# Kernel tuning notes

Measured on AMD Instinct MI355X. Metric: run time of the kernel, lower is better.

## Reference

```python
import jax, jax.numpy as jnp
import numpy as np

N_IN = 1024
N_OUT = 1024
BATCH = 8192
N_GRID = 10  # grid_points = linspace(-1, 1, 10); 9 segments
LN_EPS = 1e-5


def setup_inputs() -> dict:
    key = jax.random.key(0)
    k = jax.random.split(key, 6)
    return {
        "x": jax.random.normal(k[0], (BATCH, N_IN), dtype=jnp.float32),
        "weights": jax.random.normal(k[1], (N_OUT, N_IN), dtype=jnp.float32) * (1.0 / np.sqrt(N_IN)),
        "biases": jax.random.normal(k[2], (N_OUT,), dtype=jnp.float32),
        "slopes": jax.random.normal(k[3], (N_OUT, N_IN, N_GRID - 1), dtype=jnp.float32) * 0.05,
        "intercepts": jax.random.normal(k[4], (N_OUT, N_IN, N_GRID - 1), dtype=jnp.float32) * 0.05,
        "prelu_weight": jnp.full((1,), 0.25, dtype=jnp.float32),
    }


def reference(x, weights, biases, slopes, intercepts, prelu_weight):
    grid = jnp.linspace(-1.0, 1.0, N_GRID, dtype=x.dtype)
    n_seg = N_GRID - 1

    # base branch: GELU (exact, matching torch nn.GELU default) then linear
    b_out = jax.nn.gelu(x, approximate=False) @ weights.T + biases  # [B, n_out]

    # segment index per (sample, input feature)
    pos = (x[..., None] - grid) >= 0  # [B, n_in, N_GRID]
    seg = jnp.clip(jnp.sum(pos.astype(jnp.int32), axis=-1) - 1, 0, n_seg - 1)  # [B, n_in]

    # Faithful to torch.gather semantics: only slopes[:, 0, :] / intercepts[:, 0, :]
    # are read (index dim-2 has size 1 -> j==0). The piecewise sum over n_in then
    # reduces to segment-sums of x and segment counts contracted with those slices.
    onehot = jax.nn.one_hot(seg, n_seg, dtype=x.dtype)  # [B, n_in, n_seg]
    seg_x = jnp.einsum('bis,bi->bs', onehot, x)          # sum of x per segment
    seg_cnt = jnp.sum(onehot, axis=1)                    # count per segment
    slopes0 = slopes[:, 0, :]        # [n_out, n_seg]
    icpt0 = intercepts[:, 0, :]      # [n_out, n_seg]
    lin = seg_x @ slopes0.T + seg_cnt @ icpt0.T          # [B, n_out]

    y = b_out + lin
    # LayerNorm over n_out, no affine
    mu = jnp.mean(y, axis=-1, keepdims=True)
    var = jnp.mean(jnp.square(y - mu), axis=-1, keepdims=True)
    yn = (y - mu) * jax.lax.rsqrt(var + LN_EPS)
    # PReLU with single shared weight
    return jnp.where(yn >= 0, yn, prelu_weight * yn)
```

## Files before the change

kernel.cpp:

```cpp
#include <hip/hip_runtime.h>
#include <hip/hip_fp8.h>

#define N_IN 1024
#define N_OUT 1024
#define BATCHN 8192

typedef __attribute__((ext_vector_type(4))) int intx4;
typedef __attribute__((ext_vector_type(8))) int intx8;
typedef __attribute__((ext_vector_type(16))) float floatx16;

__device__ __forceinline__ unsigned int pk4_e4m3(float a, float b, float c,
                                                 float d) {
  int w = __builtin_amdgcn_cvt_pk_fp8_f32(a, b, 0, false);
  w = __builtin_amdgcn_cvt_pk_fp8_f32(c, d, w, true);
  return (unsigned int)w;
}
__device__ __forceinline__ float gelu_fast(float v) {
  float e = __builtin_amdgcn_exp2f(-2.4554443f * v);
  return v * __builtin_amdgcn_rcpf(1.0f + e);
}

#define ASYNC_CP16(gp, lp)                                                     \
  __builtin_amdgcn_global_load_lds(                                            \
      (const __attribute__((address_space(1))) unsigned int*)(gp),             \
      (__attribute__((address_space(3))) unsigned int*)(lp), 16, 0, 0)

__global__ __launch_bounds__(256) void prep_all(const float* __restrict__ x,
                                                unsigned char* __restrict__ g8,
                                                float2* __restrict__ seg2g,
                                                const float* __restrict__ W,
                                                unsigned char* __restrict__ Wb8,
                                                const float* __restrict__ slopes,
                                                const float* __restrict__ icpts,
                                                float* __restrict__ slt,
                                                float* __restrict__ ict) {
  const int b = blockIdx.x, t = threadIdx.x;
  if (b < BATCHN / 4) {
    const int lane = t & 63, w = t >> 6;
    const int r = b * 4 + w;
    const float* xr = x + (long)r * N_IN;
    unsigned int* grow = (unsigned int*)(g8 + (long)r * N_IN);
    const int sw = r & 7;
    float cumx[8], totx = 0.f;
    unsigned int cnt[8];
#pragma unroll
    for (int s = 0; s < 8; ++s) { cnt[s] = 0u; cumx[s] = 0.f; }
#pragma unroll
    for (int jc = 0; jc < 4; ++jc) {
      float4 v4 = ((const float4*)xr)[lane + 64 * jc];
      float vs[4] = {v4.x, v4.y, v4.z, v4.w};
      float gs[4];
#pragma unroll
      for (int e = 0; e < 4; ++e) {
        float v = vs[e];
        gs[e] = gelu_fast(v) * 4.0f;
        totx += v;
#pragma unroll
        for (int k = 0; k < 8; ++k) {
          bool m = v >= (-1.0f + (float)(k + 1) * (2.0f / 9.0f));
          cumx[k] += m ? v : 0.0f;
          cnt[k] += (unsigned int)__popcll(__ballot(m));
        }
      }
      const unsigned int pk = pk4_e4m3(gs[0], gs[1], gs[2], gs[3]);
      const int d = lane + 64 * jc;
      grow[(((d >> 2) ^ sw) << 2) | (d & 3)] = pk;
    }
#pragma unroll
    for (int off = 32; off > 0; off >>= 1) {
      totx += __shfl_xor(totx, off);
#pragma unroll
      for (int s = 0; s < 8; ++s) cumx[s] += __shfl_xor(cumx[s], off);
    }
    if (lane == 0) {
      seg2g[r * 9 + 0] = make_float2(totx - cumx[0], (float)(1024 - (int)cnt[0]));
#pragma unroll
      for (int s = 1; s < 8; ++s)
        seg2g[r * 9 + s] = make_float2(cumx[s - 1] - cumx[s],
                                       (float)((int)cnt[s - 1] - (int)cnt[s]));
      seg2g[r * 9 + 8] = make_float2(cumx[7], (float)cnt[7]);
    }
  } else if (b < BATCHN / 4 + N_OUT) {
    const int o = b - BATCHN / 4;
    float4 v = ((const float4*)(W + o * N_IN))[t];
    unsigned int pk =
        pk4_e4m3(v.x * 16.0f, v.y * 16.0f, v.z * 16.0f, v.w * 16.0f);
    const int kc = t >> 4;
    const int lh = (t >> 3) & 1;
    const int sec = (t >> 2) & 1;
    const int off = (t & 3) * 4;
    const int lane = lh * 32 + (o & 31);
    *(unsigned int*)(Wb8 + kc * 65536 + (o >> 5) * 2048 + sec * 1024 +
                     lane * 16 + off) = pk;
  } else {
    const int gb = b - (BATCHN / 4 + N_OUT);
    const int o = gb * 16 + (t >> 4);
    const int s = t & 15;
    if (s < 9) {
      slt[s * N_OUT + o] = slopes[(long)o * 9216 + s];
      ict[s * N_OUT + o] = icpts[(long)o * 9216 + s];
    }
  }
}

__global__ __launch_bounds__(1024) void gemm_ln(
    const unsigned char* __restrict__ g8, const unsigned char* __restrict__ Wb8,
    const float* __restrict__ biases, const float* __restrict__ slt,
    const float* __restrict__ ict, const float* __restrict__ prelu_w,
    const float2* __restrict__ seg2g, float* __restrict__ out) {
  __shared__ unsigned char lA[32 * 1024];
  __shared__ float2 seg2f[288];
  __shared__ float2 red[16][32];
  __shared__ float2 rowstat[32];

  const int t = threadIdx.x;
  const int lane = t & 63, w = t >> 6;
  const int l31 = lane & 31, lh = lane >> 5;
  const int r0 = blockIdx.x * 32;

#pragma unroll
  for (int j = 0; j < 2; ++j) {
    const int sg = t + 1024 * j;
    ASYNC_CP16(g8 + (long)r0 * 1024 + sg * 16, &lA[sg * 16]);
  }
  if (t < 288) seg2f[t] = seg2g[r0 * 9 + t];
  __syncthreads();

  const int nb = w * 64;
  floatx16 acc[2] = {};
  const unsigned char* aRow = lA + l31 * 1024;
  const int asw = l31 & 7;
  const unsigned char* bBase = Wb8 + (w * 2) * 2048 + lane * 16;

#define LOAD_A(ko, AF)                                                         \
  {                                                                            \
    const int c0 = ((ko) >> 4) + lh * 2;                                       \
    intx4 lo = *(const intx4*)(aRow + ((c0 ^ asw) << 4));                      \
    intx4 hi = *(const intx4*)(aRow + (((c0 + 1) ^ asw) << 4));                \
    AF[0] = lo[0]; AF[1] = lo[1]; AF[2] = lo[2]; AF[3] = lo[3];                \
    AF[4] = hi[0]; AF[5] = hi[1]; AF[6] = hi[2]; AF[7] = hi[3];                \
  }
#define LOAD_B(kc, ni, BF)                                                     \
  {                                                                            \
    const unsigned char* bp = bBase + (kc) * 65536 + (ni) * 2048;              \
    intx4 lo = *(const intx4*)bp;                                              \
    intx4 hi = *(const intx4*)(bp + 1024);                                     \
    BF[0] = lo[0]; BF[1] = lo[1]; BF[2] = lo[2]; BF[3] = lo[3];                \
    BF[4] = hi[0]; BF[5] = hi[1]; BF[6] = hi[2]; BF[7] = hi[3];                \
  }

  const int rot = ((blockIdx.x >> 3) & 7) * 2;
  for (int kt0 = 0; kt0 < 16; kt0 += 2) {
    const int kt = (kt0 + rot) & 15;
    intx8 a0, a1, b0[2], b1[2];
    LOAD_A(kt * 64, a0);
    LOAD_A(kt * 64 + 64, a1);
#pragma unroll
    for (int ni = 0; ni < 2; ++ni) LOAD_B(kt, ni, b0[ni]);
#pragma unroll
    for (int ni = 0; ni < 2; ++ni) LOAD_B(kt + 1, ni, b1[ni]);
    __builtin_amdgcn_s_setprio(1);
#pragma unroll
    for (int ni = 0; ni < 2; ++ni)
      acc[ni] = __builtin_amdgcn_mfma_scale_f32_32x32x64_f8f6f4(
          a0, b0[ni], acc[ni], 0, 0, 0, 0x7D7D7D7Du , 0,
          0x7B7B7B7Bu );
#pragma unroll
    for (int ni = 0; ni < 2; ++ni)
      acc[ni] = __builtin_amdgcn_mfma_scale_f32_32x32x64_f8f6f4(
          a1, b1[ni], acc[ni], 0, 0, 0, 0x7D7D7D7Du, 0, 0x7B7B7B7Bu);
    __builtin_amdgcn_s_setprio(0);
  }

  float bb[2], cs[2][9], ci[2][9];
#pragma unroll
  for (int ni = 0; ni < 2; ++ni) {
    const int c = nb + ni * 32 + l31;
    bb[ni] = biases[c];
#pragma unroll
    for (int s = 0; s < 9; ++s) {
      cs[ni][s] = slt[s * N_OUT + c];
      ci[ni][s] = ict[s * N_OUT + c];
    }
  }

#pragma unroll
  for (int rg = 0; rg < 16; ++rg) {
    const int rl = (rg & 3) + 8 * (rg >> 2) + 4 * lh;
    float2 sp[9];
#pragma unroll
    for (int s = 0; s < 9; ++s) sp[s] = seg2f[rl * 9 + s];
    float ssum = 0.f, qsum = 0.f;
#pragma unroll
    for (int ni = 0; ni < 2; ++ni) {
      float y = acc[ni][rg] + bb[ni];
#pragma unroll
      for (int s = 0; s < 9; ++s) y += sp[s].x * cs[ni][s] + sp[s].y * ci[ni][s];
      acc[ni][rg] = y;
      ssum += y;
      qsum += y * y;
    }
#pragma unroll
    for (int off = 16; off > 0; off >>= 1) {
      ssum += __shfl_xor(ssum, off);
      qsum += __shfl_xor(qsum, off);
    }
    if (l31 == 0) red[w][rl] = make_float2(ssum, qsum);
  }
  __syncthreads();
  if (t < 32) {
    float s = 0.f, q = 0.f;
#pragma unroll
    for (int wv = 0; wv < 16; ++wv) {
      float2 p = red[wv][t];
      s += p.x;
      q += p.y;
    }
    const float mu = s * (1.0f / 1024.0f);
    const float rstd = rsqrtf(q * (1.0f / 1024.0f) - mu * mu + 1e-5f);
    rowstat[t] = make_float2(mu, rstd);
  }
  const float pw = prelu_w[0];
  __syncthreads();
#pragma unroll
  for (int rg = 0; rg < 16; ++rg) {
    const int rl = (rg & 3) + 8 * (rg >> 2) + 4 * lh;
    const float2 ms = rowstat[rl];
    float* orow = out + (r0 + rl) * N_OUT;
#pragma unroll
    for (int ni = 0; ni < 2; ++ni) {
      float z = (acc[ni][rg] - ms.x) * ms.y;
      z = z >= 0.f ? z : pw * z;
      __builtin_nontemporal_store(z, &orow[nb + ni * 32 + l31]);
    }
  }
}

extern "C" void kernel_launch(void* const* d_in, const int* in_sizes, int n_in,
                              void* d_out, int out_size, void* d_ws, size_t ws_size,
                              hipStream_t stream) {
  const float* x = (const float*)d_in[0];
  const float* W = (const float*)d_in[1];
  const float* biases = (const float*)d_in[2];
  const float* slopes = (const float*)d_in[3];
  const float* icpts = (const float*)d_in[4];
  const float* prelu_w = (const float*)d_in[5];
  float* out = (float*)d_out;

  char* ws = (char*)d_ws;
  unsigned char* Wb8 = (unsigned char*)ws;
  float* slt = (float*)(ws + (2u << 20));
  float* ict = (float*)(ws + (2u << 20) + (64u << 10));
  unsigned char* g8 = (unsigned char*)(ws + (4u << 20));
  float2* seg2g = (float2*)(ws + (12u << 20));

  prep_all<<<BATCHN / 4 + N_OUT + 64, 256, 0, stream>>>(
      x, g8, seg2g, W, Wb8, slopes, icpts, slt, ict);
  gemm_ln<<<BATCHN / 32, 1024, 0, stream>>>(g8, Wb8, biases, slt, ict, prelu_w,
                                            seg2g, out);
}
```

Measured before the change: 165.8 us.

## Software-pipeline weight fragment loads across K-steps and prefetch before the LDS barrier

Restructures the GEMM main loop so the B (weight) fragments for the next K-chunk load into a second register set while the current chunk's MFMAs run. The first B fragments are now issued before the async A-tile copy and barrier, so global latency overlaps the LDS staging. The K rotation now covers every chunk offset rather than only even ones, and an amdgpu_waves_per_eu(4,4) hint caps register use for the occupancy implied by 1024-thread blocks. In exchange, live registers rise and the prefetch depth is only one step, so the compiler may spill or reorder differently.

```diff
diff --git a/kernel.cpp b/kernel.cpp
--- a/kernel.cpp
+++ b/kernel.cpp
@@ -103,7 +103,8 @@
   }
 }
 
-__global__ __launch_bounds__(1024) void gemm_ln(
+__global__ __launch_bounds__(1024)
+__attribute__((amdgpu_waves_per_eu(4, 4))) void gemm_ln(
     const unsigned char* __restrict__ g8, const unsigned char* __restrict__ Wb8,
     const float* __restrict__ biases, const float* __restrict__ slt,
     const float* __restrict__ ict, const float* __restrict__ prelu_w,
@@ -118,16 +119,7 @@
   const int l31 = lane & 31, lh = lane >> 5;
   const int r0 = blockIdx.x * 32;
 
-#pragma unroll
-  for (int j = 0; j < 2; ++j) {
-    const int sg = t + 1024 * j;
-    ASYNC_CP16(g8 + (long)r0 * 1024 + sg * 16, &lA[sg * 16]);
-  }
-  if (t < 288) seg2f[t] = seg2g[r0 * 9 + t];
-  __syncthreads();
-
   const int nb = w * 64;
-  floatx16 acc[2] = {};
   const unsigned char* aRow = lA + l31 * 1024;
   const int asw = l31 & 7;
   const unsigned char* bBase = Wb8 + (w * 2) * 2048 + lane * 16;
@@ -148,27 +140,43 @@
     BF[0] = lo[0]; BF[1] = lo[1]; BF[2] = lo[2]; BF[3] = lo[3];                \
     BF[4] = hi[0]; BF[5] = hi[1]; BF[6] = hi[2]; BF[7] = hi[3];                \
   }
-
-  const int rot = ((blockIdx.x >> 3) & 7) * 2;
-  for (int kt0 = 0; kt0 < 16; kt0 += 2) {
-    const int kt = (kt0 + rot) & 15;
-    intx8 a0, a1, b0[2], b1[2];
-    LOAD_A(kt * 64, a0);
-    LOAD_A(kt * 64 + 64, a1);
-#pragma unroll
-    for (int ni = 0; ni < 2; ++ni) LOAD_B(kt, ni, b0[ni]);
-#pragma unroll
-    for (int ni = 0; ni < 2; ++ni) LOAD_B(kt + 1, ni, b1[ni]);
+#define MFMA(AF, BF, C)                                                        \
+  __builtin_amdgcn_mfma_scale_f32_32x32x64_f8f6f4(                             \
+      AF, BF, C, 0, 0, 0, 0x7D7D7D7Du , 0, 0x7B7B7B7Bu )
+
+  const int rot = (blockIdx.x >> 3) & 15;
+  intx8 a0, a1, bA0, bA1, bB0, bB1;
+  LOAD_B(rot, 0, bA0);
+  LOAD_B(rot, 1, bA1);
+#pragma unroll
+  for (int j = 0; j < 2; ++j) {
+    const int sg = t + 1024 * j;
+    ASYNC_CP16(g8 + (long)r0 * 1024 + sg * 16, &lA[sg * 16]);
+  }
+  if (t < 288) seg2f[t] = seg2g[r0 * 9 + t];
+  __syncthreads();
+
+  floatx16 acc[2] = {};
+#pragma unroll
+  for (int j = 0; j < 16; j += 2) {
+    const int k0 = (j + rot) & 15;
+    const int k1 = (j + 1 + rot) & 15;
+    const int k2 = (j + 2 + rot) & 15;
+    LOAD_A(k0 * 64, a0);
+    LOAD_B(k1, 0, bB0);
+    LOAD_B(k1, 1, bB1);
     __builtin_amdgcn_s_setprio(1);
-#pragma unroll
-    for (int ni = 0; ni < 2; ++ni)
-      acc[ni] = __builtin_amdgcn_mfma_scale_f32_32x32x64_f8f6f4(
-          a0, b0[ni], acc[ni], 0, 0, 0, 0x7D7D7D7Du , 0,
-          0x7B7B7B7Bu );
-#pragma unroll
-    for (int ni = 0; ni < 2; ++ni)
-      acc[ni] = __builtin_amdgcn_mfma_scale_f32_32x32x64_f8f6f4(
-          a1, b1[ni], acc[ni], 0, 0, 0, 0x7D7D7D7Du, 0, 0x7B7B7B7Bu);
+    acc[0] = MFMA(a0, bA0, acc[0]);
+    acc[1] = MFMA(a0, bA1, acc[1]);
+    __builtin_amdgcn_s_setprio(0);
+    LOAD_A(k1 * 64, a1);
+    if (j < 14) {
+      LOAD_B(k2, 0, bA0);
+      LOAD_B(k2, 1, bA1);
+    }
+    __builtin_amdgcn_s_setprio(1);
+    acc[0] = MFMA(a1, bB0, acc[0]);
+    acc[1] = MFMA(a1, bB1, acc[1]);
     __builtin_amdgcn_s_setprio(0);
   }
 
```

New measurement: 165.6 us. Within noise of the previous version (-0.1%).

## Double-buffer W and activation k-tiles through LDS with async prefetch

Applied to the files above, without the earlier changes.

The GEMM main loop now stages each 64-wide k-tile of the FP8 weight matrix and the matching activation slice into one of two large LDS buffers, using async global-to-LDS copies issued two tiles ahead. Previously the weight fragments were read straight from global memory and the whole 32-row activation block was loaded once into LDS. The prep kernel's activation layout is changed to a k-tile-major, 4-way XOR-swizzled layout so each tile is one contiguous 2 KB chunk. The aim is to hide global latency behind MFMA work. In exchange it adds a block-wide barrier per k-tile and roughly 132 KB of LDS per block, which limits occupancy to one block per CU.

```diff
diff --git a/kernel.cpp b/kernel.cpp
--- a/kernel.cpp
+++ b/kernel.cpp
@@ -39,8 +39,9 @@
     const int lane = t & 63, w = t >> 6;
     const int r = b * 4 + w;
     const float* xr = x + (long)r * N_IN;
-    unsigned int* grow = (unsigned int*)(g8 + (long)r * N_IN);
-    const int sw = r & 7;
+    unsigned int* g32 = (unsigned int*)g8;
+    const int rb = r >> 5, rl = r & 31, sw3 = rl & 3;
+    const unsigned int rowbase = ((unsigned int)rb << 13) + (rl << 4);
     float cumx[8], totx = 0.f;
     unsigned int cnt[8];
 #pragma unroll
@@ -64,7 +65,10 @@
       }
       const unsigned int pk = pk4_e4m3(gs[0], gs[1], gs[2], gs[3]);
       const int d = lane + 64 * jc;
-      grow[(((d >> 2) ^ sw) << 2) | (d & 3)] = pk;
+      const int kt = d >> 4;
+      const int c = (d >> 2) & 3;
+      const int wd = d & 3;
+      g32[rowbase + (kt << 9) + ((c ^ sw3) << 2) + wd] = pk;
     }
 #pragma unroll
     for (int off = 32; off > 0; off >>= 1) {
@@ -108,7 +112,7 @@
     const float* __restrict__ biases, const float* __restrict__ slt,
     const float* __restrict__ ict, const float* __restrict__ prelu_w,
     const float2* __restrict__ seg2g, float* __restrict__ out) {
-  __shared__ unsigned char lA[32 * 1024];
+  __shared__ unsigned char pool[2][67584];
   __shared__ float2 seg2f[288];
   __shared__ float2 red[16][32];
   __shared__ float2 rowstat[32];
@@ -117,58 +121,58 @@
   const int lane = t & 63, w = t >> 6;
   const int l31 = lane & 31, lh = lane >> 5;
   const int r0 = blockIdx.x * 32;
-
-#pragma unroll
-  for (int j = 0; j < 2; ++j) {
-    const int sg = t + 1024 * j;
-    ASYNC_CP16(g8 + (long)r0 * 1024 + sg * 16, &lA[sg * 16]);
-  }
+  const int rot = (blockIdx.x >> 3) & 15;
+
+#define STAGE(p, kte)                                                          \
+  {                                                                            \
+    const unsigned char* bsrc = Wb8 + (kte) * 65536;                           \
+    _Pragma("unroll") for (int j = 0; j < 4; ++j) {                            \
+      const int sg = t + 1024 * j;                                             \
+      ASYNC_CP16(bsrc + sg * 16, &pool[p][sg * 16]);                           \
+    }                                                                          \
+    if (t < 128)                                                               \
+      ASYNC_CP16(g8 + ((long)blockIdx.x << 15) + (kte) * 2048 + t * 16,        \
+                 &pool[p][65536 + t * 16]);                                    \
+  }
+#define MFMA(AF, BF, C)                                                        \
+  __builtin_amdgcn_mfma_scale_f32_32x32x64_f8f6f4(                             \
+      AF, BF, C, 0, 0, 0, 0x7D7D7D7Du , 0, 0x7B7B7B7Bu )
+
+  STAGE(0, rot);
+  STAGE(1, (rot + 1) & 15);
   if (t < 288) seg2f[t] = seg2g[r0 * 9 + t];
   __syncthreads();
 
   const int nb = w * 64;
   floatx16 acc[2] = {};
-  const unsigned char* aRow = lA + l31 * 1024;
-  const int asw = l31 & 7;
-  const unsigned char* bBase = Wb8 + (w * 2) * 2048 + lane * 16;
-
-#define LOAD_A(ko, AF)                                                         \
-  {                                                                            \
-    const int c0 = ((ko) >> 4) + lh * 2;                                       \
-    intx4 lo = *(const intx4*)(aRow + ((c0 ^ asw) << 4));                      \
-    intx4 hi = *(const intx4*)(aRow + (((c0 + 1) ^ asw) << 4));                \
-    AF[0] = lo[0]; AF[1] = lo[1]; AF[2] = lo[2]; AF[3] = lo[3];                \
-    AF[4] = hi[0]; AF[5] = hi[1]; AF[6] = hi[2]; AF[7] = hi[3];                \
-  }
-#define LOAD_B(kc, ni, BF)                                                     \
-  {                                                                            \
-    const unsigned char* bp = bBase + (kc) * 65536 + (ni) * 2048;              \
-    intx4 lo = *(const intx4*)bp;                                              \
-    intx4 hi = *(const intx4*)(bp + 1024);                                     \
-    BF[0] = lo[0]; BF[1] = lo[1]; BF[2] = lo[2]; BF[3] = lo[3];                \
-    BF[4] = hi[0]; BF[5] = hi[1]; BF[6] = hi[2]; BF[7] = hi[3];                \
-  }
-
-  const int rot = ((blockIdx.x >> 3) & 7) * 2;
-  for (int kt0 = 0; kt0 < 16; kt0 += 2) {
-    const int kt = (kt0 + rot) & 15;
-    intx8 a0, a1, b0[2], b1[2];
-    LOAD_A(kt * 64, a0);
-    LOAD_A(kt * 64 + 64, a1);
-#pragma unroll
-    for (int ni = 0; ni < 2; ++ni) LOAD_B(kt, ni, b0[ni]);
-#pragma unroll
-    for (int ni = 0; ni < 2; ++ni) LOAD_B(kt + 1, ni, b1[ni]);
+  const int sw3 = l31 & 3;
+#pragma unroll
+  for (int kt = 0; kt < 16; ++kt) {
+    const int p = kt & 1;
+    intx8 aF, bf0, bf1;
+    {
+      const unsigned char* ab = &pool[p][65536] + l31 * 64;
+      intx4 lo = *(const intx4*)(ab + (((lh * 2) ^ sw3) << 4));
+      intx4 hi = *(const intx4*)(ab + (((lh * 2 + 1) ^ sw3) << 4));
+      aF[0] = lo[0]; aF[1] = lo[1]; aF[2] = lo[2]; aF[3] = lo[3];
+      aF[4] = hi[0]; aF[5] = hi[1]; aF[6] = hi[2]; aF[7] = hi[3];
+    }
+    {
+      const unsigned char* bp = &pool[p][(2 * w) * 2048] + lane * 16;
+      intx4 lo = *(const intx4*)bp;
+      intx4 hi = *(const intx4*)(bp + 1024);
+      bf0[0] = lo[0]; bf0[1] = lo[1]; bf0[2] = lo[2]; bf0[3] = lo[3];
+      bf0[4] = hi[0]; bf0[5] = hi[1]; bf0[6] = hi[2]; bf0[7] = hi[3];
+      lo = *(const intx4*)(bp + 2048);
+      hi = *(const intx4*)(bp + 3072);
+      bf1[0] = lo[0]; bf1[1] = lo[1]; bf1[2] = lo[2]; bf1[3] = lo[3];
+      bf1[4] = hi[0]; bf1[5] = hi[1]; bf1[6] = hi[2]; bf1[7] = hi[3];
+    }
+    __syncthreads();
+    if (kt < 14) STAGE(p, (kt + 2 + rot) & 15);
     __builtin_amdgcn_s_setprio(1);
-#pragma unroll
-    for (int ni = 0; ni < 2; ++ni)
-      acc[ni] = __builtin_amdgcn_mfma_scale_f32_32x32x64_f8f6f4(
-          a0, b0[ni], acc[ni], 0, 0, 0, 0x7D7D7D7Du , 0,
-          0x7B7B7B7Bu );
-#pragma unroll
-    for (int ni = 0; ni < 2; ++ni)
-      acc[ni] = __builtin_amdgcn_mfma_scale_f32_32x32x64_f8f6f4(
-          a1, b1[ni], acc[ni], 0, 0, 0, 0x7D7D7D7Du, 0, 0x7B7B7B7Bu);
+    acc[0] = MFMA(aF, bf0, acc[0]);
+    acc[1] = MFMA(aF, bf1, acc[1]);
     __builtin_amdgcn_s_setprio(0);
   }
 
```

Result: slower. 170.2 us (+2.7%).
